# Performance work log

Measured on AMD Instinct MI355X. Metric: run time of the kernel, lower is better.

Reference implementation:

```python
import jax, jax.numpy as jnp
import numpy as np

# Padded-CSR SparseLinear: in=out=4096, sparsity=0.9, padding_ratio=0.2
IN_F = 4096
OUT_F = 4096
B = 8192          # flattened leading batch dims
SPARSITY = 0.9
PAD_RATIO = 0.2
NNZ = int(round(IN_F * (1.0 - SPARSITY)))      # 410 live cols per output row
CAP = int(NNZ * (1.0 + PAD_RATIO))             # 492 padded row capacity


def setup_inputs() -> dict:
    key = jax.random.key(0)
    k1, k2, k3, k4 = jax.random.split(key, 4)
    bound = 1.0 / np.sqrt(IN_F)
    x = jax.random.normal(k1, (B, IN_F), dtype=jnp.float32)
    # column indices per padded slot; padded slots point at col 0 with value 0
    col_idx = jax.random.randint(k2, (OUT_F, CAP), 0, IN_F)
    pad_mask = (jnp.arange(CAP) < NNZ).astype(jnp.float32)  # zero out padding slots
    values = jax.random.uniform(k3, (OUT_F, CAP), jnp.float32, -bound, bound) * pad_mask
    bias = jax.random.uniform(k4, (OUT_F,), jnp.float32, -bound, bound)
    return {"x": x, "values": values, "col_idx": col_idx, "bias": bias}


def reference(x, values, col_idx, bias):
    # y[b, o] = sum_k values[o, k] * x[b, col_idx[o, k]] + bias[o]
    # Scan over the padded row-capacity dim so the live intermediate is only [B, OUT_F].
    def step(acc, slot):
        v, c = slot                    # v: [OUT_F] values, c: [OUT_F] column indices
        return acc + x[:, c] * v[None, :], None
    y0 = jnp.zeros((x.shape[0], values.shape[0]), dtype=x.dtype)
    y, _ = jax.lax.scan(step, y0, (values.T, col_idx.T))
    return y + bias[None, :]
```

## Files before the change

### kernel.cpp

```cpp
#include <hip/hip_runtime.h>
#include <hip/hip_bf16.h>
#include <stdint.h>

#define IN_F   4096
#define OUT_F  4096
#define BATCH  8192
#define CAP    492

typedef __bf16 v8bf __attribute__((ext_vector_type(8)));
typedef float  v4f  __attribute__((ext_vector_type(4)));

__global__ __launch_bounds__(256) void convert_x_kernel(
    const float* __restrict__ X, v8bf* __restrict__ Xb)
{
    const size_t i = (size_t)blockIdx.x * 256 + threadIdx.x;
    const float* p = X + i * 8;
    v8bf o;
    #pragma unroll
    for (int j = 0; j < 8; ++j) o[j] = (__bf16)p[j];
    Xb[i] = o;
}

__global__ __launch_bounds__(256) void densify_kernel(
    const float* __restrict__ values,
    const int* __restrict__ col_idx,
    __hip_bfloat16* __restrict__ W)
{
    __shared__ float rowf[2 * IN_F];
    const int t = threadIdx.x;

    #pragma unroll
    for (int i = 0; i < (2 * IN_F) / 256; ++i)
        rowf[t + i * 256] = 0.0f;
    __syncthreads();

    const int r    = t >> 7;
    const int j    = t & 127;
    const int o    = blockIdx.x * 2 + r;
    const int base = o * CAP;
    for (int k = j; k < CAP; k += 128) {
        float v = values[base + k];
        int   c = col_idx[base + k];
        atomicAdd(&rowf[r * IN_F + c], v);
    }
    __syncthreads();

    __hip_bfloat162* W2 = reinterpret_cast<__hip_bfloat162*>(W) + (size_t)blockIdx.x * IN_F;
    #pragma unroll
    for (int i = 0; i < IN_F / 256; ++i) {
        int idx = t + i * 256;
        __hip_bfloat162 h2;
        h2.x = __float2bfloat16(rowf[2 * idx]);
        h2.y = __float2bfloat16(rowf[2 * idx + 1]);
        W2[idx] = h2;
    }
}

__global__ __launch_bounds__(256) void gemm_bias_kernel(
    const __hip_bfloat16* __restrict__ X,
    const __hip_bfloat16* __restrict__ W,
    const float* __restrict__ bias,
    float* __restrict__ Y)
{
    __shared__ uint4 smem[2048];

    const int t    = threadIdx.x;
    const int wave = t >> 6;
    const int lane = t & 63;
    const int ml   = lane & 15;
    const int q    = lane >> 4;
    const int wm   = wave >> 1;
    const int wn   = wave & 1;
    const int bm   = blockIdx.y;
    const int bn   = blockIdx.x;

    const int trow = t >> 3;
    const int k8s  = (t & 7) ^ (trow & 7);
    const __hip_bfloat16* gA = X + (size_t)(bm * 128 + trow) * IN_F + k8s * 8;
    const __hip_bfloat16* gB = W + (size_t)(bn * 128 + trow) * IN_F + k8s * 8;

    const int xr = ml & 7;
    int aBase[4], bBase[4];
    #pragma unroll
    for (int mb = 0; mb < 4; ++mb) aBase[mb] = (wm * 64 + mb * 16 + ml) * 8;
    #pragma unroll
    for (int nf = 0; nf < 4; ++nf) bBase[nf] = 1024 + (wn * 64 + nf * 16 + ml) * 8;

    v4f acc[4][4] = {};

    for (int kt = 0; kt < IN_F / 64; ++kt) {
        uint4 ra[4], rb[4];
        #pragma unroll
        for (int c = 0; c < 4; ++c) {
            ra[c] = *reinterpret_cast<const uint4*>(gA + (size_t)kt * 64 + (size_t)c * 32 * IN_F);
            rb[c] = *reinterpret_cast<const uint4*>(gB + (size_t)kt * 64 + (size_t)c * 32 * IN_F);
        }
        #pragma unroll
        for (int c = 0; c < 4; ++c) {
            smem[c * 256 + t]        = ra[c];
            smem[1024 + c * 256 + t] = rb[c];
        }
        __syncthreads();

        #pragma unroll
        for (int j = 0; j < 2; ++j) {
            const int ko = (j * 4 + q) ^ xr;
            v8bf a[4], b[4];
            #pragma unroll
            for (int mb = 0; mb < 4; ++mb)
                a[mb] = *reinterpret_cast<const v8bf*>(&smem[aBase[mb] + ko]);
            #pragma unroll
            for (int nf = 0; nf < 4; ++nf)
                b[nf] = *reinterpret_cast<const v8bf*>(&smem[bBase[nf] + ko]);
            #pragma unroll
            for (int mb = 0; mb < 4; ++mb)
                #pragma unroll
                for (int nf = 0; nf < 4; ++nf)
                    acc[mb][nf] = __builtin_amdgcn_mfma_f32_16x16x32_bf16(
                        a[mb], b[nf], acc[mb][nf], 0, 0, 0);
        }
        __syncthreads();
    }

    float bf[4];
    #pragma unroll
    for (int nf = 0; nf < 4; ++nf)
        bf[nf] = bias[bn * 128 + wn * 64 + nf * 16 + ml];

    #pragma unroll
    for (int mb = 0; mb < 4; ++mb) {
        const int row0 = bm * 128 + wm * 64 + mb * 16 + q * 4;
        #pragma unroll
        for (int nf = 0; nf < 4; ++nf) {
            const int col = bn * 128 + wn * 64 + nf * 16 + ml;
            float* yp = Y + (size_t)row0 * OUT_F + col;
            #pragma unroll
            for (int r = 0; r < 4; ++r)
                yp[(size_t)r * OUT_F] = acc[mb][nf][r] + bf[nf];
        }
    }
}

__global__ __launch_bounds__(256) void fallback_kernel(
    const float* __restrict__ x,
    const float* __restrict__ values,
    const int* __restrict__ col_idx,
    const float* __restrict__ bias,
    float* __restrict__ y)
{
    __shared__ float xrow[IN_F];
    const int b = blockIdx.y;
    const int t = threadIdx.x;
    for (int i = t; i < IN_F; i += 256)
        xrow[i] = x[(size_t)b * IN_F + i];
    __syncthreads();
    const int o    = blockIdx.x * 256 + t;
    const int base = o * CAP;
    float acc = bias[o];
    for (int k = 0; k < CAP; ++k)
        acc += values[base + k] * xrow[col_idx[base + k]];
    y[(size_t)b * OUT_F + o] = acc;
}

extern "C" void kernel_launch(void* const* d_in, const int* in_sizes, int n_in,
                              void* d_out, int out_size, void* d_ws, size_t ws_size,
                              hipStream_t stream)
{
    const float* x      = (const float*)d_in[0];
    const float* values = (const float*)d_in[1];
    const int*   colidx = (const int*)d_in[2];
    const float* bias   = (const float*)d_in[3];
    float*       y      = (float*)d_out;

    const size_t w_bytes  = (size_t)OUT_F * IN_F * sizeof(__hip_bfloat16);
    const size_t xb_bytes = (size_t)BATCH * IN_F * sizeof(__hip_bfloat16);
    if (ws_size >= w_bytes + xb_bytes) {
        __hip_bfloat16* W  = (__hip_bfloat16*)d_ws;
        __hip_bfloat16* Xb = (__hip_bfloat16*)((char*)d_ws + w_bytes);

        convert_x_kernel<<<(BATCH * IN_F) / (256 * 8), 256, 0, stream>>>(x, (v8bf*)Xb);
        densify_kernel<<<OUT_F / 2, 256, 0, stream>>>(values, colidx, W);
        dim3 grid(OUT_F / 128, BATCH / 128);
        gemm_bias_kernel<<<grid, 256, 0, stream>>>(Xb, W, bias, y);
    } else {
        dim3 grid(OUT_F / 256, BATCH);
        fallback_kernel<<<grid, 256, 0, stream>>>(x, values, colidx, bias, y);
    }
}
```

Measured before the change: 509.6 us.

## Merge prep kernels and load GEMM tiles directly into LDS

Merges the x-to-bf16 conversion and weight densification into one launch that splits work by block index, with the conversion now using float4 loads. In the GEMM main loop, the global-to-register-to-LDS staging is replaced with global_load_lds direct-to-LDS loads of 16 bytes per lane. The goal is to cut one launch and the register round trip and VGPR pressure of tile staging. It relies on the per-lane LDS placement of the direct loads matching the previous swizzled layout, and the conversion blocks in the merged launch now also reserve the large shared buffer.

```diff
diff --git a/kernel.cpp b/kernel.cpp
--- a/kernel.cpp
+++ b/kernel.cpp
@@ -8,26 +8,36 @@
 #define CAP    492
 
 typedef __bf16 v8bf __attribute__((ext_vector_type(8)));
+typedef __bf16 v4bf __attribute__((ext_vector_type(4)));
 typedef float  v4f  __attribute__((ext_vector_type(4)));
 
-__global__ __launch_bounds__(256) void convert_x_kernel(
-    const float* __restrict__ X, v8bf* __restrict__ Xb)
-{
-    const size_t i = (size_t)blockIdx.x * 256 + threadIdx.x;
-    const float* p = X + i * 8;
-    v8bf o;
-    #pragma unroll
-    for (int j = 0; j < 8; ++j) o[j] = (__bf16)p[j];
-    Xb[i] = o;
-}
+#define GPTR(p) ((const __attribute__((address_space(1))) void*)(p))
+#define LPTR(p) ((__attribute__((address_space(3))) void*)(p))
 
-__global__ __launch_bounds__(256) void densify_kernel(
+#define CONV_BLOCKS ((BATCH * IN_F / 4) / 256)
+#define DENS_BLOCKS (OUT_F / 2)
+
+__global__ __launch_bounds__(256) void prep_kernel(
+    const float* __restrict__ X,
+    v4bf* __restrict__ Xb,
     const float* __restrict__ values,
     const int* __restrict__ col_idx,
     __hip_bfloat16* __restrict__ W)
 {
     __shared__ float rowf[2 * IN_F];
     const int t = threadIdx.x;
+
+    if (blockIdx.x < CONV_BLOCKS) {
+        const size_t i = (size_t)blockIdx.x * 256 + t;
+        const float4 f = reinterpret_cast<const float4*>(X)[i];
+        v4bf o;
+        o[0] = (__bf16)f.x; o[1] = (__bf16)f.y;
+        o[2] = (__bf16)f.z; o[3] = (__bf16)f.w;
+        Xb[i] = o;
+        return;
+    }
+
+    const int bid = blockIdx.x - CONV_BLOCKS;
 
     #pragma unroll
     for (int i = 0; i < (2 * IN_F) / 256; ++i)
@@ -36,7 +46,7 @@
 
     const int r    = t >> 7;
     const int j    = t & 127;
-    const int o    = blockIdx.x * 2 + r;
+    const int o    = bid * 2 + r;
     const int base = o * CAP;
     for (int k = j; k < CAP; k += 128) {
         float v = values[base + k];
@@ -45,7 +55,7 @@
     }
     __syncthreads();
 
-    __hip_bfloat162* W2 = reinterpret_cast<__hip_bfloat162*>(W) + (size_t)blockIdx.x * IN_F;
+    __hip_bfloat162* W2 = reinterpret_cast<__hip_bfloat162*>(W) + (size_t)bid * IN_F;
     #pragma unroll
     for (int i = 0; i < IN_F / 256; ++i) {
         int idx = t + i * 256;
@@ -89,17 +99,16 @@
     v4f acc[4][4] = {};
 
     for (int kt = 0; kt < IN_F / 64; ++kt) {
-        uint4 ra[4], rb[4];
+        const __hip_bfloat16* pa = gA + kt * 64;
+        const __hip_bfloat16* pb = gB + kt * 64;
         #pragma unroll
-        for (int c = 0; c < 4; ++c) {
-            ra[c] = *reinterpret_cast<const uint4*>(gA + (size_t)kt * 64 + (size_t)c * 32 * IN_F);
-            rb[c] = *reinterpret_cast<const uint4*>(gB + (size_t)kt * 64 + (size_t)c * 32 * IN_F);
-        }
+        for (int c = 0; c < 4; ++c)
+            __builtin_amdgcn_global_load_lds(GPTR(pa + (size_t)c * 32 * IN_F),
+                                             LPTR(&smem[c * 256 + wave * 64]), 16, 0, 0);
         #pragma unroll
-        for (int c = 0; c < 4; ++c) {
-            smem[c * 256 + t]        = ra[c];
-            smem[1024 + c * 256 + t] = rb[c];
-        }
+        for (int c = 0; c < 4; ++c)
+            __builtin_amdgcn_global_load_lds(GPTR(pb + (size_t)c * 32 * IN_F),
+                                             LPTR(&smem[1024 + c * 256 + wave * 64]), 16, 0, 0);
         __syncthreads();
 
         #pragma unroll
@@ -178,8 +187,8 @@
         __hip_bfloat16* W  = (__hip_bfloat16*)d_ws;
         __hip_bfloat16* Xb = (__hip_bfloat16*)((char*)d_ws + w_bytes);
 
-        convert_x_kernel<<<(BATCH * IN_F) / (256 * 8), 256, 0, stream>>>(x, (v8bf*)Xb);
-        densify_kernel<<<OUT_F / 2, 256, 0, stream>>>(values, colidx, W);
+        prep_kernel<<<CONV_BLOCKS + DENS_BLOCKS, 256, 0, stream>>>(
+            x, (v4bf*)Xb, values, colidx, W);
         dim3 grid(OUT_F / 128, BATCH / 128);
         gemm_bias_kernel<<<grid, 256, 0, stream>>>(Xb, W, bias, y);
     } else {
```

Result: faster. 475.2 us (-6.7%).
